# Kernel tuning notes

Measured on AMD Instinct MI355X. Metric: run time of the kernel, lower is better.

## Reference

```python
import jax, jax.numpy as jnp
import numpy as np

E = 384      # EMBEDDING_SIZE
DFF = 1536
H = 6        # NUM_HEADS
D = E // H   # ATTN_DIM_SIZE = 64
T = 256      # SEQ_LEN
L = 6        # NUM_BLOCKS
V = 65       # VOCAB_SIZE
NPOS = 10000.0
B = 128


def _pos_encoding():
    i = jnp.arange(T, dtype=jnp.float32)[:, None]
    k = jnp.arange(E // 2, dtype=jnp.float32)[None, :]
    ang = i / jnp.power(NPOS, 2.0 * k / E)   # [T, E/2]
    pe = jnp.zeros((T, E), dtype=jnp.float32)
    pe = pe.at[:, 0::2].set(jnp.sin(ang))
    pe = pe.at[:, 1::2].set(jnp.cos(ang))
    return pe


def setup_inputs() -> dict:
    key = jax.random.key(0)
    ks = jax.random.split(key, 24)
    s = 0.02
    n = lambda k, shp: (jax.random.normal(k, shp, dtype=jnp.float32) * s)
    inp = {
        'tokens': jax.random.randint(ks[0], (B, T), 0, V),
        'pos_enc': _pos_encoding(),
        'emb': n(ks[1], (V, E)),
        # stacked per-layer params [L, ...]; weights stored as (in, out)
        'Wq': n(ks[2], (L, E, E)), 'bq': jnp.zeros((L, E)),
        'Wk': n(ks[3], (L, E, E)), 'bk': jnp.zeros((L, E)),
        'Wv': n(ks[4], (L, E, E)), 'bv': jnp.zeros((L, E)),
        'Wo': n(ks[5], (L, E, E)), 'bo': jnp.zeros((L, E)),
        'ln1_g': jnp.ones((L, E)), 'ln1_b': jnp.zeros((L, E)),
        'W1': n(ks[6], (L, E, DFF)), 'c1': jnp.zeros((L, DFF)),
        'W2': n(ks[7], (L, DFF, E)), 'c2': jnp.zeros((L, E)),
        'ln2_g': jnp.ones((L, E)), 'ln2_b': jnp.zeros((L, E)),
        'Wl': n(ks[8], (E, V)), 'bl': jnp.zeros((V,)),
    }
    return inp


def _layer_norm(x, g, b, eps=1e-5):
    mu = jnp.mean(x, axis=-1, keepdims=True)
    var = jnp.mean((x - mu) ** 2, axis=-1, keepdims=True)
    return (x - mu) * jax.lax.rsqrt(var + eps) * g + b


def _decoder(tokens, pos_enc, emb, Wq, bq, Wk, bk, Wv, bv, Wo, bo,
             ln1_g, ln1_b, W1, c1, W2, c2, ln2_g, ln2_b, Wl, bl):
    b_, t_ = tokens.shape
    x = emb[tokens] + pos_enc[None, :t_, :]            # [B,T,E]
    causal = jnp.tril(jnp.ones((t_, t_), dtype=bool)) # tril mask
    scale = D ** (-0.5)

    def block(x, p):
        (wq, bq_, wk, bk_, wv, bv_, wo, bo_, g1, be1, w1, c1_, w2, c2_, g2, be2) = p
        h = _layer_norm(x, g1, be1)
        q = (h @ wq + bq_).reshape(b_, t_, H, D)
        k = (h @ wk + bk_).reshape(b_, t_, H, D)
        v = (h @ wv + bv_).reshape(b_, t_, H, D)
        scores = jnp.einsum('bqhd,bkhd->bhqk', q, k) * scale
        scores = jnp.where(causal[None, None], scores, -jnp.inf)
        attn = jax.nn.softmax(scores, axis=-1)
        o = jnp.einsum('bhqk,bkhd->bqhd', attn, v).reshape(b_, t_, E)
        x = x + (o @ wo + bo_)
        h2 = _layer_norm(x, g2, be2)
        x = x + (jax.nn.relu(h2 @ w1 + c1_) @ w2 + c2_)
        return x, None

    params = (Wq, bq, Wk, bk, Wv, bv, Wo, bo, ln1_g, ln1_b, W1, c1, W2, c2, ln2_g, ln2_b)
    x, _ = jax.lax.scan(block, x, params)
    return x @ Wl + bl                                 # [B,T,V]


def reference(tokens, pos_enc, emb, Wq, bq, Wk, bk, Wv, bv, Wo, bo,
              ln1_g, ln1_b, W1, c1, W2, c2, ln2_g, ln2_b, Wl, bl):
    return _decoder(tokens, pos_enc, emb, Wq, bq, Wk, bk, Wv, bv, Wo, bo,
                    ln1_g, ln1_b, W1, c1, W2, c2, ln2_g, ln2_b, Wl, bl)
```

## Files before the change

### kernel.cpp

```cpp
#include <hip/hip_runtime.h>
#include <hip/hip_bf16.h>
#include <stdint.h>

constexpr int E   = 384;
constexpr int DFF = 1536;
constexpr int NH  = 6;
constexpr int HD  = 64;
constexpr int T   = 256;
constexpr int NL  = 6;
constexpr int NV  = 65;
constexpr int BB  = 128;
constexpr int MTOT = BB * T;
constexpr int CB  = 32;

typedef __bf16 bf16;
typedef __attribute__((ext_vector_type(8))) __bf16 bf16x8;
typedef __attribute__((ext_vector_type(4))) float floatx4;

#define GBM 128
#define GBN 128
#define GBK 64

template <int MODE>
__global__ __launch_bounds__(256) void k_gemm(
    const bf16* __restrict__ A, int lda,
    const bf16* __restrict__ Bf,
    const float* __restrict__ bias,
    void* __restrict__ Cv, void* __restrict__ Cv2, int ldc,
    int Mtiles, int Ntiles, int Nvalid, int K,
    int relu)
{
    __shared__ __align__(16) bf16 As[2 * GBM * GBK];

    int nb = gridDim.x;
    int per = nb >> 3;
    int bphys = blockIdx.x;
    int bid = (bphys & 7) * per + (bphys >> 3);

    int nt = bid % Ntiles;
    int mt = bid / Ntiles;

    const bf16* Ab = A + (long)mt * GBM * lda;

    int tid = threadIdx.x;
    int lane = tid & 63;
    int wid = tid >> 6;
    int wm = wid >> 1, wn = wid & 1;
    int lq = lane >> 4, lr = lane & 15;

    int srow = tid >> 3;
    int skc  = (tid & 7) * 8;

    const bf16* Arow = Ab + (long)srow * lda + skc;
    const long a2 = 32 * (long)lda;

    char* AsB = (char*)As;
    int wcol = ((tid & 7) * 16) ^ ((srow & 7) << 4);
    char* wp0 = AsB + srow * 128 + wcol;

    int nk = K / GBK;
    int nks = K / 32;
    const bf16* Bq = Bf + ((long)(nt * 8 + wn * 4) * nks) * 512 + lane * 8;

    floatx4 zero = {0.f, 0.f, 0.f, 0.f};
    floatx4 acc[4][4];
#pragma unroll
    for (int i = 0; i < 4; i++)
#pragma unroll
        for (int j = 0; j < 4; j++) acc[i][j] = zero;

    const char* rp0 = AsB + (wm * 64 + lr) * 128;
    int rx0 = (lq * 16) ^ ((lr & 7) << 4);

    bf16x8 ra[4];
#pragma unroll
    for (int g = 0; g < 4; g++) ra[g] = *(const bf16x8*)(Arow + g * a2);
#pragma unroll
    for (int g = 0; g < 4; g++) *(bf16x8*)(wp0 + g * 4096) = ra[g];
    if (nk > 1) {
#pragma unroll
        for (int g = 0; g < 4; g++) ra[g] = *(const bf16x8*)(Arow + g * a2 + GBK);
    }
    __syncthreads();

    for (int ki = 0; ki < nk; ki++) {
        int ib = ki & 1;
        bf16x8 bb[8];
#pragma unroll
        for (int ni = 0; ni < 4; ni++)
#pragma unroll
            for (int kh = 0; kh < 2; kh++)
                bb[ni * 2 + kh] =
                    *(const bf16x8*)(Bq + ((long)ni * nks + 2 * ki + kh) * 512);
        if (ki + 1 < nk) {
            char* wp = wp0 + (1 - ib) * 16384;
#pragma unroll
            for (int g = 0; g < 4; g++) *(bf16x8*)(wp + g * 4096) = ra[g];
        }
        if (ki + 2 < nk) {
            long koff = (long)(ki + 2) * GBK;
#pragma unroll
            for (int g = 0; g < 4; g++)
                ra[g] = *(const bf16x8*)(Arow + g * a2 + koff);
        }
        const char* rp = rp0 + ib * 16384;

        bf16x8 af[4];
#pragma unroll
        for (int mi = 0; mi < 4; mi++)
            af[mi] = *(const bf16x8*)(rp + mi * 2048 + rx0);
#pragma unroll
        for (int mi = 0; mi < 4; mi++)
#pragma unroll
            for (int ni = 0; ni < 4; ni++)
                acc[mi][ni] = __builtin_amdgcn_mfma_f32_16x16x32_bf16(
                    af[mi], bb[ni * 2], acc[mi][ni], 0, 0, 0);
#pragma unroll
        for (int mi = 0; mi < 4; mi++)
            af[mi] = *(const bf16x8*)(rp + mi * 2048 + (rx0 ^ 64));
#pragma unroll
        for (int mi = 0; mi < 4; mi++)
#pragma unroll
            for (int ni = 0; ni < 4; ni++)
                acc[mi][ni] = __builtin_amdgcn_mfma_f32_16x16x32_bf16(
                    af[mi], bb[ni * 2 + 1], acc[mi][ni], 0, 0, 0);
        __syncthreads();
    }

    int m0 = mt * GBM, n0 = nt * GBN;
#pragma unroll
    for (int mi = 0; mi < 4; mi++) {
#pragma unroll
        for (int ni = 0; ni < 4; ni++) {
            int colL = n0 + wn * 64 + ni * 16 + lr;
#pragma unroll
            for (int r = 0; r < 4; r++) {
                int rowL = m0 + wm * 64 + mi * 16 + lq * 4 + r;
                float val = acc[mi][ni][r];
                if (MODE == 5) {
                    val += bias[colL];
                    if (colL < 768) {
                        bf16* Cp = (bf16*)Cv;
                        Cp[(long)rowL * 768 + colL] = (bf16)val;
                    } else {
                        bf16* Cp = (bf16*)Cv2;
                        long addr = (long)(rowL >> 8) * (E * T) + (long)(colL - 768) * T + (rowL & 255);
                        Cp[addr] = (bf16)val;
                    }
                } else if (MODE == 1) {
                    bf16* Cp = (bf16*)Cv;
                    long idx = (long)rowL * ldc + colL;
                    Cp[idx] = (bf16)((float)Cp[idx] + val + bias[colL]);
                } else if (MODE == 4) {
                    if (colL < Nvalid) {
                        float* Cp = (float*)Cv;
                        Cp[(long)rowL * ldc + colL] = val + bias[colL];
                    }
                } else {
                    if (colL < Nvalid) {
                        if (bias) val += bias[colL];
                        if (relu) val = fmaxf(val, 0.f);
                        bf16* Cp = (bf16*)Cv;
                        Cp[(long)rowL * ldc + colL] = (bf16)val;
                    }
                }
            }
        }
    }
}

__global__ __launch_bounds__(256) void k_attn(
    const bf16* __restrict__ qk, const bf16* __restrict__ vt,
    bf16* __restrict__ o)
{
    int nb = gridDim.x;
    int per = nb >> 3;
    int bphys = blockIdx.x;
    int bid = (bphys & 7) * per + (bphys >> 3);

    int qt = bid & 3; bid >>= 2;
    int h = bid % NH; int b = bid / NH;
    int tid = threadIdx.x;
    int lane = tid & 63;
    int w = tid >> 6;
    int lq = lane >> 4;
    int lr = lane & 15;

    __shared__ __align__(16) bf16 Ks[256 * 72];
    __shared__ __align__(16) bf16 Vs[64 * 264];

    const bf16* qbase = qk + (long)(b * T + qt * 64 + w * 16) * 768 + h * 64;
    const bf16* kbase = qk + (long)(b * T) * 768 + 384 + h * 64;
    const bf16* vbase = vt + ((long)b * E + h * 64) * T;

#pragma unroll
    for (int i = 0; i < 8; i++) {
        int idx = i * 256 + tid;
        int row = idx >> 3, off = (idx & 7) * 8;
        *(bf16x8*)(&Ks[row * 72 + off]) = *(const bf16x8*)(kbase + (long)row * 768 + off);
    }
#pragma unroll
    for (int i = 0; i < 8; i++) {
        int idx = i * 256 + tid;
        int row = idx >> 5, off = (idx & 31) * 8;
        *(bf16x8*)(&Vs[row * 264 + off]) = *(const bf16x8*)(vbase + (long)row * 256 + off);
    }

    bf16x8 aq0 = *(const bf16x8*)(qbase + (long)lr * 768 + lq * 8);
    bf16x8 aq1 = *(const bf16x8*)(qbase + (long)lr * 768 + 32 + lq * 8);

    __syncthreads();

    const int ntmax = qt * 4 + 3;
    floatx4 zero = {0.f, 0.f, 0.f, 0.f};
    floatx4 s[16];
#pragma unroll
    for (int nt = 0; nt < 16; nt++) s[nt] = zero;

#pragma unroll
    for (int nt = 0; nt < 16; nt++) {
        if (nt <= ntmax) {
            const bf16* kp = &Ks[(nt * 16 + lr) * 72 + lq * 8];
            bf16x8 b0 = *(const bf16x8*)(kp);
            bf16x8 b1 = *(const bf16x8*)(kp + 32);
            s[nt] = __builtin_amdgcn_mfma_f32_16x16x32_bf16(aq0, b0, s[nt], 0, 0, 0);
            s[nt] = __builtin_amdgcn_mfma_f32_16x16x32_bf16(aq1, b1, s[nt], 0, 0, 0);
        }
    }

    int trow0 = qt * 64 + w * 16 + lq * 4;
    float m4[4] = {-3e38f, -3e38f, -3e38f, -3e38f};
#pragma unroll
    for (int nt = 0; nt < 16; nt++) {
        if (nt <= ntmax) {
            int tc = nt * 16 + lr;
#pragma unroll
            for (int r = 0; r < 4; r++) {
                float v = s[nt][r] * 0.125f;
                if (tc > trow0 + r) v = -3e38f;
                s[nt][r] = v;
                m4[r] = fmaxf(m4[r], v);
            }
        }
    }
#pragma unroll
    for (int r = 0; r < 4; r++) {
#pragma unroll
        for (int off = 1; off < 16; off <<= 1)
            m4[r] = fmaxf(m4[r], __shfl_xor(m4[r], off, 64));
    }

    float l4[4] = {0.f, 0.f, 0.f, 0.f};
#pragma unroll
    for (int nt = 0; nt < 16; nt++) {
        if (nt <= ntmax) {
#pragma unroll
            for (int r = 0; r < 4; r++) {
                float pv = __expf(s[nt][r] - m4[r]);
                l4[r] += pv;
                s[nt][r] = pv;
            }
        }
    }
#pragma unroll
    for (int r = 0; r < 4; r++) {
#pragma unroll
        for (int off = 1; off < 16; off <<= 1)
            l4[r] += __shfl_xor(l4[r], off, 64);
    }

    __syncthreads();

    bf16* P = Ks + w * (16 * 264);
#pragma unroll
    for (int nt = 0; nt < 16; nt++) {
        if (nt <= ntmax) {
#pragma unroll
            for (int r = 0; r < 4; r++)
                P[(lq * 4 + r) * 264 + nt * 16 + lr] = (bf16)s[nt][r];
        }
    }

    floatx4 oacc[4];
#pragma unroll
    for (int nd = 0; nd < 4; nd++) oacc[nd] = zero;
    const int kkmax = 2 * (qt + 1);
#pragma unroll
    for (int kk = 0; kk < 8; kk++) {
        if (kk < kkmax) {
            bf16x8 ap = *(const bf16x8*)(&P[lr * 264 + kk * 32 + lq * 8]);
#pragma unroll
            for (int nd = 0; nd < 4; nd++) {
                bf16x8 bv = *(const bf16x8*)(&Vs[(nd * 16 + lr) * 264 + kk * 32 + lq * 8]);
                oacc[nd] = __builtin_amdgcn_mfma_f32_16x16x32_bf16(ap, bv, oacc[nd], 0, 0, 0);
            }
        }
    }

#pragma unroll
    for (int r = 0; r < 4; r++) {
        float inv = 1.0f / l4[r];
        long rowg = (long)b * T + trow0 + r;
#pragma unroll
        for (int nd = 0; nd < 4; nd++) {
            o[rowg * E + h * 64 + nd * 16 + lr] = (bf16)(oacc[nd][r] * inv);
        }
    }
}

__global__ void k_ln(const bf16* __restrict__ x, const float* __restrict__ g,
                     const float* __restrict__ b, bf16* __restrict__ h) {
    int row = blockIdx.x * 4 + (threadIdx.x >> 6);
    int lane = threadIdx.x & 63;
    const bf16* xr = x + (long)row * E;
    float v[6];
    float s = 0.f;
#pragma unroll
    for (int i = 0; i < 6; i++) { v[i] = (float)xr[lane + 64 * i]; s += v[i]; }
#pragma unroll
    for (int o = 1; o < 64; o <<= 1) s += __shfl_xor(s, o, 64);
    float mu = s * (1.0f / E);
    float q = 0.f;
#pragma unroll
    for (int i = 0; i < 6; i++) { float d = v[i] - mu; q += d * d; }
#pragma unroll
    for (int o = 1; o < 64; o <<= 1) q += __shfl_xor(q, o, 64);
    float rs = rsqrtf(q * (1.0f / E) + 1e-5f);
    bf16* hr = h + (long)row * E;
#pragma unroll
    for (int i = 0; i < 6; i++) {
        int c = lane + 64 * i;
        hr[c] = (bf16)((v[i] - mu) * rs * g[c] + b[c]);
    }
}

__global__ void k_transpose_frag(const float* __restrict__ W, bf16* __restrict__ Wf,
                                 int K, int N, int NPAD) {
    long idx = (long)blockIdx.x * 256 + threadIdx.x;
    long per = (long)NPAD * K;
    int l = (int)(idx / per);
    long r = idx - (long)l * per;
    int j = (int)(r & 7); r >>= 3;
    int lane = (int)(r & 63); r >>= 6;
    int nks = K / 32;
    int ks = (int)(r % nks);
    int c16 = (int)(r / nks);
    int col = c16 * 16 + (lane & 15);
    int k = ks * 32 + (lane >> 4) * 8 + j;
    Wf[idx] = (col < N) ? (bf16)W[((long)l * K + k) * N + col] : (bf16)0.0f;
}

__global__ void k_transpose_qkv_frag(const float* __restrict__ Wq, const float* __restrict__ Wk,
                                     const float* __restrict__ Wv, bf16* __restrict__ Wf) {
    long idx = (long)blockIdx.x * 256 + threadIdx.x;
    long per = (long)1152 * E;
    int l = (int)(idx / per);
    long r = idx - (long)l * per;
    int j = (int)(r & 7); r >>= 3;
    int lane = (int)(r & 63); r >>= 6;
    int nks = E / 32;
    int ks = (int)(r % nks);
    int c16 = (int)(r / nks);
    int col = c16 * 16 + (lane & 15);
    int k = ks * 32 + (lane >> 4) * 8 + j;
    const float* src;
    int cc;
    if (col < 384)      { src = Wq; cc = col; }
    else if (col < 768) { src = Wk; cc = col - 384; }
    else                { src = Wv; cc = col - 768; }
    Wf[idx] = (bf16)src[((long)l * E + k) * E + cc];
}

__global__ void k_bias_qkv(const float* __restrict__ bq, const float* __restrict__ bk,
                           const float* __restrict__ bv, float* __restrict__ bqkv) {
    int idx = blockIdx.x * 256 + threadIdx.x;
    int l = idx / 1152;
    int j = idx - l * 1152;
    const float* src;
    int jj;
    if (j < 384)      { src = bq; jj = j; }
    else if (j < 768) { src = bk; jj = j - 384; }
    else              { src = bv; jj = j - 768; }
    bqkv[idx] = src[l * E + jj];
}

__global__ void k_embed(const int* __restrict__ tokens, const float* __restrict__ pos,
                        const float* __restrict__ emb, bf16* __restrict__ x) {
    long idx = (long)blockIdx.x * 256 + threadIdx.x;
    int e = (int)(idx % E);
    long bt = idx / E;
    int t = (int)(bt % T);
    int tok = tokens[bt];
    x[idx] = (bf16)(emb[(long)tok * E + e] + pos[(long)t * E + e]);
}

extern "C" void kernel_launch(void* const* d_in, const int* in_sizes, int n_in,
                              void* d_out, int out_size, void* d_ws, size_t ws_size,
                              hipStream_t stream) {
    const int*   tokens = (const int*)d_in[0];
    const float* pos  = (const float*)d_in[1];
    const float* emb  = (const float*)d_in[2];
    const float* Wq   = (const float*)d_in[3];
    const float* bq   = (const float*)d_in[4];
    const float* Wk   = (const float*)d_in[5];
    const float* bk   = (const float*)d_in[6];
    const float* Wv   = (const float*)d_in[7];
    const float* bv   = (const float*)d_in[8];
    const float* Wo   = (const float*)d_in[9];
    const float* bo   = (const float*)d_in[10];
    const float* g1   = (const float*)d_in[11];
    const float* be1  = (const float*)d_in[12];
    const float* W1   = (const float*)d_in[13];
    const float* c1   = (const float*)d_in[14];
    const float* W2   = (const float*)d_in[15];
    const float* c2   = (const float*)d_in[16];
    const float* g2   = (const float*)d_in[17];
    const float* be2  = (const float*)d_in[18];
    const float* Wl   = (const float*)d_in[19];
    const float* bl   = (const float*)d_in[20];

    char* p = (char*)d_ws;
    bf16* x  = (bf16*)p;   p += (long)MTOT * E * 2;
    bf16* h  = (bf16*)p;   p += (long)MTOT * E * 2;
    bf16* qk = (bf16*)p;   p += (long)MTOT * 768 * 2;
    bf16* vt = (bf16*)p;   p += (long)BB * E * T * 2;
    bf16* SP = (bf16*)p;   p += (long)CB * NH * T * T * 2;
    bf16* WqkvF = (bf16*)p; p += (long)NL * 1152 * E * 2;
    bf16* WoF = (bf16*)p;  p += (long)NL * E * E * 2;
    bf16* W1F = (bf16*)p;  p += (long)NL * DFF * E * 2;
    bf16* W2F = (bf16*)p;  p += (long)NL * E * DFF * 2;
    bf16* WlF = (bf16*)p;  p += (long)128 * E * 2;
    float* bqkv = (float*)p; p += (long)NL * 1152 * 4;
    bf16* mid = qk;
    bf16* o   = h;
    (void)SP;

    k_transpose_qkv_frag<<<(NL * 1152 * E) / 256, 256, 0, stream>>>(Wq, Wk, Wv, WqkvF);
    k_transpose_frag<<<(NL * E * E) / 256, 256, 0, stream>>>(Wo, WoF, E, E, E);
    k_transpose_frag<<<(NL * DFF * E) / 256, 256, 0, stream>>>(W1, W1F, E, DFF, DFF);
    k_transpose_frag<<<(NL * E * DFF) / 256, 256, 0, stream>>>(W2, W2F, DFF, E, E);
    k_transpose_frag<<<(128 * E) / 256, 256, 0, stream>>>(Wl, WlF, E, NV, 128);
    k_bias_qkv<<<(NL * 1152) / 256, 256, 0, stream>>>(bq, bk, bv, bqkv);

    k_embed<<<(MTOT * E) / 256, 256, 0, stream>>>(tokens, pos, emb, x);

    for (int l = 0; l < NL; l++) {
        k_ln<<<MTOT / 4, 256, 0, stream>>>(x, g1 + l * E, be1 + l * E, h);
        k_gemm<5><<<256 * 9, 256, 0, stream>>>(h, E, WqkvF + (long)l * 1152 * E,
                                               bqkv + l * 1152, qk, vt, 0,
                                               256, 9, 1152, E, 0);
        k_attn<<<BB * NH * 4, 256, 0, stream>>>(qk, vt, o);
        k_gemm<1><<<256 * 3, 256, 0, stream>>>(o, E, WoF + (long)l * E * E,
                                               bo + l * E, x, nullptr, E,
                                               256, 3, E, E, 0);
        k_ln<<<MTOT / 4, 256, 0, stream>>>(x, g2 + l * E, be2 + l * E, h);
        k_gemm<0><<<256 * 12, 256, 0, stream>>>(h, E, W1F + (long)l * DFF * E,
                                                c1 + l * DFF, mid, nullptr, DFF,
                                                256, 12, DFF, E, 1);
        k_gemm<1><<<256 * 3, 256, 0, stream>>>(mid, DFF, W2F + (long)l * E * DFF,
                                               c2 + l * E, x, nullptr, E,
                                               256, 3, E, DFF, 0);
    }

    k_gemm<4><<<256 * 1, 256, 0, stream>>>(x, E, WlF,
                                           bl, d_out, nullptr, NV,
                                           256, 1, NV, E, 0);
}
```

Baseline: 2.018 ms.

## Use 512-thread GEMM blocks with swapped MFMA operands for vectorized epilogue stores

After: 1.774 ms. -12.1%, faster.

```diff
diff --git a/kernel.cpp b/kernel.cpp
--- a/kernel.cpp
+++ b/kernel.cpp
@@ -15,14 +15,165 @@
 
 typedef __bf16 bf16;
 typedef __attribute__((ext_vector_type(8))) __bf16 bf16x8;
+typedef __attribute__((ext_vector_type(4))) __bf16 bf16x4;
 typedef __attribute__((ext_vector_type(4))) float floatx4;
 
 #define GBM 128
 #define GBN 128
 #define GBK 64
 
+template <int MODE, int SWAP>
+__device__ __forceinline__ void gemm_body(
+    char* AsB,
+    const bf16* __restrict__ A, int lda,
+    const bf16* __restrict__ Bf,
+    const float* __restrict__ bias,
+    void* __restrict__ Cv, void* __restrict__ Cv2, int ldc,
+    int nt, int mt, int Nvalid, int K, int relu)
+{
+    int tid = threadIdx.x;
+    int lane = tid & 63;
+    int wid = tid >> 6;
+    int wm = wid >> 2, wn = wid & 3;
+    int lq = lane >> 4, lr = lane & 15;
+
+    const bf16* Ab = A + (long)mt * GBM * lda;
+
+    int srow = tid >> 3;
+    int skc  = (tid & 7) * 8;
+    const bf16* Arow = Ab + (long)srow * lda + skc;
+    const long a2 = 64 * (long)lda;
+
+    int wcol = ((tid & 7) * 16) ^ ((srow & 7) << 4);
+    char* wp0 = AsB + srow * 128 + wcol;
+
+    int nk = K / GBK;
+    int nks = K / 32;
+    const bf16* Bq = Bf + ((long)(nt * 8 + wn * 2) * nks) * 512 + lane * 8;
+
+    floatx4 zero = {0.f, 0.f, 0.f, 0.f};
+    floatx4 acc[4][2];
+#pragma unroll
+    for (int i = 0; i < 4; i++)
+#pragma unroll
+        for (int j = 0; j < 2; j++) acc[i][j] = zero;
+
+    const char* rp0 = AsB + (wm * 64 + lr) * 128;
+    int rx0 = (lq * 16) ^ ((lr & 7) << 4);
+
+    bf16x8 ra[2];
+    ra[0] = *(const bf16x8*)(Arow);
+    ra[1] = *(const bf16x8*)(Arow + a2);
+    *(bf16x8*)(wp0)        = ra[0];
+    *(bf16x8*)(wp0 + 8192) = ra[1];
+    if (nk > 1) {
+        ra[0] = *(const bf16x8*)(Arow + GBK);
+        ra[1] = *(const bf16x8*)(Arow + a2 + GBK);
+    }
+    __syncthreads();
+
+    for (int ki = 0; ki < nk; ki++) {
+        int ib = ki & 1;
+        bf16x8 bb[4];
+#pragma unroll
+        for (int ni = 0; ni < 2; ni++)
+#pragma unroll
+            for (int kh = 0; kh < 2; kh++)
+                bb[ni * 2 + kh] =
+                    *(const bf16x8*)(Bq + ((long)ni * nks + 2 * ki + kh) * 512);
+        if (ki + 1 < nk) {
+            char* wp = wp0 + (1 - ib) * 16384;
+            *(bf16x8*)(wp)        = ra[0];
+            *(bf16x8*)(wp + 8192) = ra[1];
+        }
+        if (ki + 2 < nk) {
+            long koff = (long)(ki + 2) * GBK;
+            ra[0] = *(const bf16x8*)(Arow + koff);
+            ra[1] = *(const bf16x8*)(Arow + a2 + koff);
+        }
+        const char* rp = rp0 + ib * 16384;
+
+        bf16x8 af[4];
+#pragma unroll
+        for (int mi = 0; mi < 4; mi++)
+            af[mi] = *(const bf16x8*)(rp + mi * 2048 + rx0);
+#pragma unroll
+        for (int mi = 0; mi < 4; mi++)
+#pragma unroll
+            for (int ni = 0; ni < 2; ni++)
+                acc[mi][ni] = SWAP
+                    ? __builtin_amdgcn_mfma_f32_16x16x32_bf16(bb[ni * 2], af[mi], acc[mi][ni], 0, 0, 0)
+                    : __builtin_amdgcn_mfma_f32_16x16x32_bf16(af[mi], bb[ni * 2], acc[mi][ni], 0, 0, 0);
+#pragma unroll
+        for (int mi = 0; mi < 4; mi++)
+            af[mi] = *(const bf16x8*)(rp + mi * 2048 + (rx0 ^ 64));
+#pragma unroll
+        for (int mi = 0; mi < 4; mi++)
+#pragma unroll
+            for (int ni = 0; ni < 2; ni++)
+                acc[mi][ni] = SWAP
+                    ? __builtin_amdgcn_mfma_f32_16x16x32_bf16(bb[ni * 2 + 1], af[mi], acc[mi][ni], 0, 0, 0)
+                    : __builtin_amdgcn_mfma_f32_16x16x32_bf16(af[mi], bb[ni * 2 + 1], acc[mi][ni], 0, 0, 0);
+        __syncthreads();
+    }
+
+    int m0 = mt * GBM, n0 = nt * GBN;
+#pragma unroll
+    for (int mi = 0; mi < 4; mi++) {
+#pragma unroll
+        for (int ni = 0; ni < 2; ni++) {
+            floatx4 v = acc[mi][ni];
+            if (SWAP) {
+                int rowL = m0 + wm * 64 + mi * 16 + lr;
+                int col0 = n0 + wn * 32 + ni * 16 + lq * 4;
+                if (MODE == 5) {
+                    bf16x4 pv;
+#pragma unroll
+                    for (int r = 0; r < 4; r++) pv[r] = (bf16)(v[r] + bias[col0 + r]);
+                    *(bf16x4*)((bf16*)Cv + (long)rowL * 768 + col0) = pv;
+                } else if (MODE == 1) {
+                    bf16* Cp = (bf16*)Cv;
+                    bf16x4* ptr = (bf16x4*)(Cp + (long)rowL * ldc + col0);
+                    bf16x4 old = *ptr;
+                    bf16x4 pv;
+#pragma unroll
+                    for (int r = 0; r < 4; r++)
+                        pv[r] = (bf16)((float)old[r] + v[r] + bias[col0 + r]);
+                    *ptr = pv;
+                } else if (MODE == 4) {
+                    float* Cp = (float*)Cv;
+#pragma unroll
+                    for (int r = 0; r < 4; r++)
+                        if (col0 + r < Nvalid)
+                            Cp[(long)rowL * ldc + col0 + r] = v[r] + bias[col0 + r];
+                } else {
+                    if (col0 < Nvalid) {
+                        bf16x4 pv;
+#pragma unroll
+                        for (int r = 0; r < 4; r++) {
+                            float x = v[r] + (bias ? bias[col0 + r] : 0.f);
+                            if (relu) x = fmaxf(x, 0.f);
+                            pv[r] = (bf16)x;
+                        }
+                        *(bf16x4*)((bf16*)Cv + (long)rowL * ldc + col0) = pv;
+                    }
+                }
+            } else {
+                int row0 = m0 + wm * 64 + mi * 16 + lq * 4;
+                int colL = n0 + wn * 32 + ni * 16 + lr;
+                float bv = bias[colL];
+                bf16x4 pv;
+#pragma unroll
+                for (int r = 0; r < 4; r++) pv[r] = (bf16)(v[r] + bv);
+                int bidx = row0 >> 8, pos = row0 & 255, e = colL - 768;
+                *(bf16x4*)((bf16*)Cv2 + (long)bidx * (E * T) + (long)e * T + pos) = pv;
+            }
+        }
+    }
+}
+
 template <int MODE>
-__global__ __launch_bounds__(256) void k_gemm(
+__global__ __launch_bounds__(512, 4) void k_gemm(
     const bf16* __restrict__ A, int lda,
     const bf16* __restrict__ Bf,
     const float* __restrict__ bias,
@@ -30,7 +181,7 @@
     int Mtiles, int Ntiles, int Nvalid, int K,
     int relu)
 {
-    __shared__ __align__(16) bf16 As[2 * GBM * GBK];
+    __shared__ __align__(16) char AsB[2 * 16384];
 
     int nb = gridDim.x;
     int per = nb >> 3;
@@ -40,133 +191,10 @@
     int nt = bid % Ntiles;
     int mt = bid / Ntiles;
 
-    const bf16* Ab = A + (long)mt * GBM * lda;
-
-    int tid = threadIdx.x;
-    int lane = tid & 63;
-    int wid = tid >> 6;
-    int wm = wid >> 1, wn = wid & 1;
-    int lq = lane >> 4, lr = lane & 15;
-
-    int srow = tid >> 3;
-    int skc  = (tid & 7) * 8;
-
-    const bf16* Arow = Ab + (long)srow * lda + skc;
-    const long a2 = 32 * (long)lda;
-
-    char* AsB = (char*)As;
-    int wcol = ((tid & 7) * 16) ^ ((srow & 7) << 4);
-    char* wp0 = AsB + srow * 128 + wcol;
-
-    int nk = K / GBK;
-    int nks = K / 32;
-    const bf16* Bq = Bf + ((long)(nt * 8 + wn * 4) * nks) * 512 + lane * 8;
-
-    floatx4 zero = {0.f, 0.f, 0.f, 0.f};
-    floatx4 acc[4][4];
-#pragma unroll
-    for (int i = 0; i < 4; i++)
-#pragma unroll
-        for (int j = 0; j < 4; j++) acc[i][j] = zero;
-
-    const char* rp0 = AsB + (wm * 64 + lr) * 128;
-    int rx0 = (lq * 16) ^ ((lr & 7) << 4);
-
-    bf16x8 ra[4];
-#pragma unroll
-    for (int g = 0; g < 4; g++) ra[g] = *(const bf16x8*)(Arow + g * a2);
-#pragma unroll
-    for (int g = 0; g < 4; g++) *(bf16x8*)(wp0 + g * 4096) = ra[g];
-    if (nk > 1) {
-#pragma unroll
-        for (int g = 0; g < 4; g++) ra[g] = *(const bf16x8*)(Arow + g * a2 + GBK);
-    }
-    __syncthreads();
-
-    for (int ki = 0; ki < nk; ki++) {
-        int ib = ki & 1;
-        bf16x8 bb[8];
-#pragma unroll
-        for (int ni = 0; ni < 4; ni++)
-#pragma unroll
-            for (int kh = 0; kh < 2; kh++)
-                bb[ni * 2 + kh] =
-                    *(const bf16x8*)(Bq + ((long)ni * nks + 2 * ki + kh) * 512);
-        if (ki + 1 < nk) {
-            char* wp = wp0 + (1 - ib) * 16384;
-#pragma unroll
-            for (int g = 0; g < 4; g++) *(bf16x8*)(wp + g * 4096) = ra[g];
-        }
-        if (ki + 2 < nk) {
-            long koff = (long)(ki + 2) * GBK;
-#pragma unroll
-            for (int g = 0; g < 4; g++)
-                ra[g] = *(const bf16x8*)(Arow + g * a2 + koff);
-        }
-        const char* rp = rp0 + ib * 16384;
-
-        bf16x8 af[4];
-#pragma unroll
-        for (int mi = 0; mi < 4; mi++)
-            af[mi] = *(const bf16x8*)(rp + mi * 2048 + rx0);
-#pragma unroll
-        for (int mi = 0; mi < 4; mi++)
-#pragma unroll
-            for (int ni = 0; ni < 4; ni++)
-                acc[mi][ni] = __builtin_amdgcn_mfma_f32_16x16x32_bf16(
-                    af[mi], bb[ni * 2], acc[mi][ni], 0, 0, 0);
-#pragma unroll
-        for (int mi = 0; mi < 4; mi++)
-            af[mi] = *(const bf16x8*)(rp + mi * 2048 + (rx0 ^ 64));
-#pragma unroll
-        for (int mi = 0; mi < 4; mi++)
-#pragma unroll
-            for (int ni = 0; ni < 4; ni++)
-                acc[mi][ni] = __builtin_amdgcn_mfma_f32_16x16x32_bf16(
-                    af[mi], bb[ni * 2 + 1], acc[mi][ni], 0, 0, 0);
-        __syncthreads();
-    }
-
-    int m0 = mt * GBM, n0 = nt * GBN;
-#pragma unroll
-    for (int mi = 0; mi < 4; mi++) {
-#pragma unroll
-        for (int ni = 0; ni < 4; ni++) {
-            int colL = n0 + wn * 64 + ni * 16 + lr;
-#pragma unroll
-            for (int r = 0; r < 4; r++) {
-                int rowL = m0 + wm * 64 + mi * 16 + lq * 4 + r;
-                float val = acc[mi][ni][r];
-                if (MODE == 5) {
-                    val += bias[colL];
-                    if (colL < 768) {
-                        bf16* Cp = (bf16*)Cv;
-                        Cp[(long)rowL * 768 + colL] = (bf16)val;
-                    } else {
-                        bf16* Cp = (bf16*)Cv2;
-                        long addr = (long)(rowL >> 8) * (E * T) + (long)(colL - 768) * T + (rowL & 255);
-                        Cp[addr] = (bf16)val;
-                    }
-                } else if (MODE == 1) {
-                    bf16* Cp = (bf16*)Cv;
-                    long idx = (long)rowL * ldc + colL;
-                    Cp[idx] = (bf16)((float)Cp[idx] + val + bias[colL]);
-                } else if (MODE == 4) {
-                    if (colL < Nvalid) {
-                        float* Cp = (float*)Cv;
-                        Cp[(long)rowL * ldc + colL] = val + bias[colL];
-                    }
-                } else {
-                    if (colL < Nvalid) {
-                        if (bias) val += bias[colL];
-                        if (relu) val = fmaxf(val, 0.f);
-                        bf16* Cp = (bf16*)Cv;
-                        Cp[(long)rowL * ldc + colL] = (bf16)val;
-                    }
-                }
-            }
-        }
-    }
+    if (MODE == 5 && nt >= 6)
+        gemm_body<5, 0>(AsB, A, lda, Bf, bias, Cv, Cv2, ldc, nt, mt, Nvalid, K, relu);
+    else
+        gemm_body<MODE, 1>(AsB, A, lda, Bf, bias, Cv, Cv2, ldc, nt, mt, Nvalid, K, relu);
 }
 
 __global__ __launch_bounds__(256) void k_attn(
@@ -446,23 +474,23 @@
 
     for (int l = 0; l < NL; l++) {
         k_ln<<<MTOT / 4, 256, 0, stream>>>(x, g1 + l * E, be1 + l * E, h);
-        k_gemm<5><<<256 * 9, 256, 0, stream>>>(h, E, WqkvF + (long)l * 1152 * E,
+        k_gemm<5><<<256 * 9, 512, 0, stream>>>(h, E, WqkvF + (long)l * 1152 * E,
                                                bqkv + l * 1152, qk, vt, 0,
                                                256, 9, 1152, E, 0);
         k_attn<<<BB * NH * 4, 256, 0, stream>>>(qk, vt, o);
-        k_gemm<1><<<256 * 3, 256, 0, stream>>>(o, E, WoF + (long)l * E * E,
+        k_gemm<1><<<256 * 3, 512, 0, stream>>>(o, E, WoF + (long)l * E * E,
                                                bo + l * E, x, nullptr, E,
                                                256, 3, E, E, 0);
         k_ln<<<MTOT / 4, 256, 0, stream>>>(x, g2 + l * E, be2 + l * E, h);
-        k_gemm<0><<<256 * 12, 256, 0, stream>>>(h, E, W1F + (long)l * DFF * E,
+        k_gemm<0><<<256 * 12, 512, 0, stream>>>(h, E, W1F + (long)l * DFF * E,
                                                 c1 + l * DFF, mid, nullptr, DFF,
                                                 256, 12, DFF, E, 1);
-        k_gemm<1><<<256 * 3, 256, 0, stream>>>(mid, DFF, W2F + (long)l * E * DFF,
+        k_gemm<1><<<256 * 3, 512, 0, stream>>>(mid, DFF, W2F + (long)l * E * DFF,
                                                c2 + l * E, x, nullptr, E,
                                                256, 3, E, DFF, 0);
     }
 
-    k_gemm<4><<<256 * 1, 256, 0, stream>>>(x, E, WlF,
+    k_gemm<4><<<256 * 1, 512, 0, stream>>>(x, E, WlF,
                                            bl, d_out, nullptr, NV,
                                            256, 1, NV, E, 0);
 }
```
